# Kernel tuning notes

Measured on AMD Instinct MI355X. Metric: run time of the kernel, lower is better.

## Reference

```python
import jax, jax.numpy as jnp
import numpy as np

N_NODES = 2048
N_EDGES = 65536
IN_CH, HID_CH, OUT_CH = 512, 256, 128
NDIM = 5
THRESHOLD = 0.5


def _gcn(x, src, dst, ew, W, b):
    # GCNConv with self-loops (weight 1): D^{-1/2}(A+I)D^{-1/2} X W + b
    n = x.shape[0]
    deg = jnp.zeros((n,), x.dtype).at[dst].add(ew) + 1.0
    dinv = 1.0 / jnp.sqrt(deg)
    h = x @ W  # [N, out]
    coef = ew * dinv[src] * dinv[dst]  # [E]
    agg = jnp.zeros_like(h).at[dst].add(h[src] * coef[:, None])
    return agg + h / deg[:, None] + b


def _class_flags(feat, thr):
    # cosine similarity -> unnormalized Laplacian -> eigengap-based class ids
    xn = feat / (jnp.linalg.norm(feat, axis=1, keepdims=True) + 1e-8)
    S = xn @ xn.T  # [N, N]
    L = jnp.diag(jnp.sum(S, axis=1)) - S
    vals = jnp.linalg.eigvalsh(jax.lax.stop_gradient(L))  # ascending (class ids are non-diff)
    gaps = jnp.diff(vals)
    return jnp.concatenate([jnp.zeros((1,), jnp.int32),
                            jnp.cumsum((gaps > thr).astype(jnp.int32))])


def _class_avg(flags, feat):
    # per-class mean features, gathered back to each node
    n = feat.shape[0]
    sums = jax.ops.segment_sum(feat, flags, num_segments=n)
    cnts = jax.ops.segment_sum(jnp.ones((n,), feat.dtype), flags, num_segments=n)
    avg = sums / jnp.maximum(cnts, 1.0)[:, None]
    return avg[flags]


def _block(prev_gcn, skip, srcs, dsts, ews, convW, convb, linW, linb, k,
           changeW=None, changeb=None):
    gcn_out, outs = [], []
    for i in range(NDIM):
        g = _gcn(prev_gcn[i], srcs[i], dsts[i], ews[i], convW[i], convb[i])
        flags = _class_flags(g, THRESHOLD)
        lin = _class_avg(flags, g) @ linW + linb
        fir = skip[i] @ changeW + changeb if changeW is not None else skip[i]
        fea = fir + k * lin  # add_class_avg_to_node_features
        outs.append(jax.nn.relu(fir + fea))
        gcn_out.append(g)
    return gcn_out, outs


def _forward(dims, edge_indices, edge_weights, convWs, convbs, linWs, linbs,
             change1_W, change1_b, change2_W, change2_b, dimension_weights, k_save):
    srcs = [edge_indices[i, 0] for i in range(NDIM)]
    dsts = [edge_indices[i, 1] for i in range(NDIM)]
    ews = [edge_weights[i] for i in range(NDIM)]
    w = dimension_weights / jnp.sum(dimension_weights)
    g, out = _block(dims, dims, srcs, dsts, ews, convWs[0], convbs[0], linWs[0], linbs[0], k_save, change1_W, change1_b)
    g, out = _block(g, out, srcs, dsts, ews, convWs[1], convbs[1], linWs[1], linbs[1], k_save, change2_W, change2_b)
    for layer in range(2, 6):
        g, out = _block(g, out, srcs, dsts, ews, convWs[layer], convbs[layer], linWs[layer], linbs[layer], k_save)
    # dimension-weighted fusion of final per-dimension outputs
    return sum(w[i] * out[i] for i in range(NDIM))


def setup_inputs() -> dict:
    key = jax.random.key(0)
    ks = iter(jax.random.split(key, 80))
    def nrm(shape, s=0.05):
        return (jax.random.normal(next(ks), shape, jnp.float32) * s)
    inp = {}
    for i in range(NDIM):
        inp[f"dim{i+1}"] = jax.random.normal(next(ks), (N_NODES, IN_CH), jnp.float32)
    inp["edge_indices"] = jax.random.randint(next(ks), (NDIM, 2, N_EDGES), 0, N_NODES, jnp.int32)
    inp["edge_weights"] = jax.random.uniform(next(ks), (NDIM, N_EDGES), jnp.float32)
    inp["non_zero"] = N_NODES
    conv_shapes = [(IN_CH, HID_CH), (HID_CH, OUT_CH)] + [(OUT_CH, OUT_CH)] * 4
    for l, (ci, co) in enumerate(conv_shapes, start=1):
        inp[f"convW{l}"] = nrm((NDIM, ci, co))
        inp[f"convb{l}"] = nrm((NDIM, co))
    lin_shapes = [HID_CH, OUT_CH, OUT_CH, OUT_CH, OUT_CH, OUT_CH]
    names = ["preLin1", "preLin2", "preLin3", "behLin1", "behLin2", "behLin3"]
    for nm, c in zip(names, lin_shapes):
        inp[f"{nm}_W"] = nrm((c, c))
        inp[f"{nm}_b"] = nrm((c,))
    inp["change1_W"] = nrm((IN_CH, HID_CH)); inp["change1_b"] = nrm((HID_CH,))
    inp["change2_W"] = nrm((HID_CH, OUT_CH)); inp["change2_b"] = nrm((OUT_CH,))
    inp["dimension_weights"] = jnp.ones((NDIM,), jnp.float32)
    inp["k_save"] = jnp.float32(0.5)
    return inp


def reference(dim1, dim2, dim3, dim4, dim5, edge_indices, edge_weights, non_zero,
              convW1, convb1, convW2, convb2, convW3, convb3, convW4, convb4,
              convW5, convb5, convW6, convb6,
              preLin1_W, preLin1_b, preLin2_W, preLin2_b, preLin3_W, preLin3_b,
              behLin1_W, behLin1_b, behLin2_W, behLin2_b, behLin3_W, behLin3_b,
              change1_W, change1_b, change2_W, change2_b, dimension_weights, k_save):
    dims = [dim1, dim2, dim3, dim4, dim5]
    convWs = [convW1, convW2, convW3, convW4, convW5, convW6]
    convbs = [convb1, convb2, convb3, convb4, convb5, convb6]
    linWs = [preLin1_W, preLin2_W, preLin3_W, behLin1_W, behLin2_W, behLin3_W]
    linbs = [preLin1_b, preLin2_b, preLin3_b, behLin1_b, behLin2_b, behLin3_b]
    return _forward(dims, edge_indices, edge_weights, convWs, convbs, linWs, linbs,
                    change1_W, change1_b, change2_W, change2_b, dimension_weights, k_save)
```

## Files before the change

kernel.cpp:

```cpp
#include <hip/hip_runtime.h>
#include <math.h>
#include <stdint.h>

#define NN 2048
#define NE 65536
#define ND 5
#define DMX 256
#define MAXB1 2048
#define SUBD 8
#define NBF (MAXB1*SUBD+1)
#define NFMAX 1536
#define MAXRUN 1536
#define NPB 4
#define COARSE_H 1.76f
#define NUDGE 2e-3f
#define THRG 0.5f

typedef float f32x16 __attribute__((ext_vector_type(16)));
typedef short s16x8 __attribute__((ext_vector_type(8)));
typedef unsigned short u16x8 __attribute__((ext_vector_type(8)));

__device__ __forceinline__ float wredSum(float v){
#pragma unroll
  for (int o=32;o>0;o>>=1) v += __shfl_down(v,o,64);
  return v;
}
__device__ __forceinline__ float wredMin(float v){
#pragma unroll
  for (int o=32;o>0;o>>=1) v = fminf(v,__shfl_down(v,o,64));
  return v;
}
__device__ __forceinline__ float wredMax(float v){
#pragma unroll
  for (int o=32;o>0;o>>=1) v = fmaxf(v,__shfl_down(v,o,64));
  return v;
}
__device__ __forceinline__ uint32_t encF(float f){
  uint32_t u = __float_as_uint(f);
  return (u & 0x80000000u) ? ~u : (u | 0x80000000u);
}
__device__ __forceinline__ float decF(uint32_t u){
  return (u & 0x80000000u) ? __uint_as_float(u ^ 0x80000000u) : __uint_as_float(~u);
}
__device__ __forceinline__ uint16_t bf16hi(float f){
  return (uint16_t)(__float_as_uint(f)>>16);
}

template<int BLK>
__device__ float bredSum(float v, float* red){
  v = wredSum(v);
  const int w = threadIdx.x >> 6;
  if ((threadIdx.x & 63) == 0) red[w] = v;
  __syncthreads();
  if (threadIdx.x == 0){
    float s = 0.f;
#pragma unroll
    for (int i=0;i<BLK/64;i++) s += red[i];
    red[0] = s;
  }
  __syncthreads();
  float r = red[0];
  __syncthreads();
  return r;
}

__global__ void k_prep(const float* __restrict__ xn, uint16_t* __restrict__ xph,
                       uint16_t* __restrict__ xpl, int co){
  const int dim = blockIdx.y;
  const int c2 = blockIdx.x;
  const int col = threadIdx.x;
  const float* x = xn + (size_t)dim*NN*co;
  const int kb = c2*8;
  u16x8 h8, l8;
#pragma unroll
  for (int j=0;j<8;j++){
    const float x0 = x[(size_t)(kb+j)*co + col];
    const uint16_t h = bf16hi(x0);
    h8[j] = h;
    l8[j] = bf16hi(x0 - __uint_as_float((uint32_t)h<<16));
  }
  const size_t o = ((size_t)dim*(NN/8) + c2)*co + col;
  reinterpret_cast<u16x8*>(xph)[o] = h8;
  reinterpret_cast<u16x8*>(xpl)[o] = l8;
}

template<int D, int BLK>
__device__ int evalNu(const uint16_t* __restrict__ xph, const uint16_t* __restrict__ xpl,
                      const float* __restrict__ a,
                      float t0, float dlt,
                      float* M, float* Pt, float* red, float* wrow,
                      float* scal, float* tOut)
{
  const int tid = threadIdx.x;
  float* fsc = scal + 16;

  float md = 1e30f;
  for (int i=tid;i<NN;i+=BLK) md = fminf(md, fabsf(a[i]-t0));
  md = wredMin(md);
  if ((tid & 63) == 0) red[tid>>6] = md;
  __syncthreads();
  if (tid == 0){
    float m2 = 1e30f;
    for (int i=0;i<BLK/64;i++) m2 = fminf(m2, red[i]);
    scal[1] = (m2 < 1e-3f) ? (t0 + dlt) : t0;
  }
  __syncthreads();
  const float t = scal[1];
  __syncthreads();

  float c = 0.f;
  for (int i=tid;i<NN;i+=BLK) c += (a[i] < t) ? 1.f : 0.f;
  float cnt = bredSum<BLK>(c, red);

  constexpr int BG  = D/64;
  constexpr int NBL = BG*(BG+1)/2;
  constexpr int SXT = 24;
  static_assert(BLK == NBL*64, "one wave per tile block");
  static_assert(4*D*SXT*2 <= (D*(D+1)/2)*4, "XT overlay fits in M");

  uint16_t* XTh = reinterpret_cast<uint16_t*>(M);
  uint16_t* XTl = XTh + D*SXT;
  uint16_t* WXh = XTl + D*SXT;
  uint16_t* WXl = WXh + D*SXT;
  const u16x8* XPH = reinterpret_cast<const u16x8*>(xph);
  const u16x8* XPL = reinterpret_cast<const u16x8*>(xpl);

  const int wv_ = tid >> 6, lane = tid & 63;
  int bi = 0, bj = 0;
  { int rem = wv_; while (rem >= BG - bi){ rem -= BG - bi; bi++; } bj = bi + rem; }
  const int colA = bi*64 + (lane & 31);
  const int colB = bj*64 + (lane & 31);
  const int kgo  = (lane >> 5) * 8;

  f32x16 acc0, acc1, acc2, acc3;
#pragma unroll
  for (int e=0;e<16;e++){ acc0[e]=0.f; acc1[e]=0.f; acc2[e]=0.f; acc3[e]=0.f; }

  if (tid < 16){
    float den = a[tid] - t;
    if (fabsf(den) < 1e-5f) den = (den < 0.f) ? -1e-5f : 1e-5f;
    wrow[tid] = 1.0f/den;
  }

  for (int k0=0; k0<NN; k0+=16){
    __syncthreads();
    const float* wcur = wrow + ((k0>>4)&1)*16;
    for (int it = tid; it < 2*D; it += BLK){
      const int kg  = it / D;
      const int col = it - kg*D;
      const u16x8 xh8 = XPH[(size_t)((k0>>3)+kg)*D + col];
      const u16x8 xl8 = XPL[(size_t)((k0>>3)+kg)*D + col];
      const float4 w0 = *reinterpret_cast<const float4*>(&wcur[kg*8]);
      const float4 w1 = *reinterpret_cast<const float4*>(&wcur[kg*8+4]);
      const float wv[8] = {w0.x,w0.y,w0.z,w0.w,w1.x,w1.y,w1.z,w1.w};
      u16x8 sph, spl;
#pragma unroll
      for (int j=0;j<8;j++){
        const float hf = __uint_as_float((uint32_t)(uint16_t)xh8[j]<<16);
        const float lf = __uint_as_float((uint32_t)(uint16_t)xl8[j]<<16);
        const float p0 = wv[j]*(hf+lf);
        const uint16_t hp = bf16hi(p0);
        sph[j] = hp;
        spl[j] = bf16hi(p0 - __uint_as_float((uint32_t)hp<<16));
      }
      const int base = col*SXT + kg*8;
      *reinterpret_cast<u16x8*>(XTh + base) = xh8;
      *reinterpret_cast<u16x8*>(XTl + base) = xl8;
      *reinterpret_cast<u16x8*>(WXh + base) = sph;
      *reinterpret_cast<u16x8*>(WXl + base) = spl;
    }
    if (tid < 16 && k0+16 < NN){
      float den = a[k0+16+tid] - t;
      if (fabsf(den) < 1e-5f) den = (den < 0.f) ? -1e-5f : 1e-5f;
      wrow[((((k0>>4)+1)&1)<<4) + tid] = 1.0f/den;
    }
    __syncthreads();
    const s16x8 ah0 = *reinterpret_cast<const s16x8*>(WXh + colA*SXT + kgo);
    const s16x8 ah1 = *reinterpret_cast<const s16x8*>(WXh + (colA+32)*SXT + kgo);
    const s16x8 al0 = *reinterpret_cast<const s16x8*>(WXl + colA*SXT + kgo);
    const s16x8 al1 = *reinterpret_cast<const s16x8*>(WXl + (colA+32)*SXT + kgo);
    const s16x8 bh0 = *reinterpret_cast<const s16x8*>(XTh + colB*SXT + kgo);
    const s16x8 bh1 = *reinterpret_cast<const s16x8*>(XTh + (colB+32)*SXT + kgo);
    const s16x8 bl0 = *reinterpret_cast<const s16x8*>(XTl + colB*SXT + kgo);
    const s16x8 bl1 = *reinterpret_cast<const s16x8*>(XTl + (colB+32)*SXT + kgo);
    acc0 = __builtin_amdgcn_mfma_f32_32x32x16_bf16(ah0, bh0, acc0, 0,0,0);
    acc1 = __builtin_amdgcn_mfma_f32_32x32x16_bf16(ah0, bh1, acc1, 0,0,0);
    acc2 = __builtin_amdgcn_mfma_f32_32x32x16_bf16(ah1, bh0, acc2, 0,0,0);
    acc3 = __builtin_amdgcn_mfma_f32_32x32x16_bf16(ah1, bh1, acc3, 0,0,0);
    acc0 = __builtin_amdgcn_mfma_f32_32x32x16_bf16(ah0, bl0, acc0, 0,0,0);
    acc1 = __builtin_amdgcn_mfma_f32_32x32x16_bf16(ah0, bl1, acc1, 0,0,0);
    acc2 = __builtin_amdgcn_mfma_f32_32x32x16_bf16(ah1, bl0, acc2, 0,0,0);
    acc3 = __builtin_amdgcn_mfma_f32_32x32x16_bf16(ah1, bl1, acc3, 0,0,0);
    acc0 = __builtin_amdgcn_mfma_f32_32x32x16_bf16(al0, bh0, acc0, 0,0,0);
    acc1 = __builtin_amdgcn_mfma_f32_32x32x16_bf16(al0, bh1, acc1, 0,0,0);
    acc2 = __builtin_amdgcn_mfma_f32_32x32x16_bf16(al1, bh0, acc2, 0,0,0);
    acc3 = __builtin_amdgcn_mfma_f32_32x32x16_bf16(al1, bh1, acc3, 0,0,0);
  }
  __syncthreads();

  {
    const int rbase = 4*(lane>>5);
#pragma unroll
    for (int q=0;q<4;q++){
      const f32x16 A = (q==0)?acc0:((q==1)?acc1:((q==2)?acc2:acc3));
      const int ta = 2*bi + (q>>1), tb = 2*bj + (q&1);
      const int bb = tb*32 + (lane & 31);
#pragma unroll
      for (int r=0;r<16;r++){
        const int aa = ta*32 + (r&3) + 8*(r>>2) + rbase;
        if (aa <= bb)
          M[aa*D - (aa*(aa-1))/2 + (bb-aa)] = ((aa==bb)?1.f:0.f) - A[r];
      }
    }
  }

  constexpr int PS = 12;
  int neg = 0;
  for (int k0=0; k0<D; k0+=8){
    const int k1 = k0+8;
    __syncthreads();
    if (tid < 64){
      if (tid == 0){
        float B[8][8];
#pragma unroll
        for (int q=0;q<8;q++){
#pragma unroll
          for (int p=0;p<=q;p++){
            const int g = k0+p;
            B[p][q] = M[g*D - (g*(g-1))/2 + (k0+q-g)];
          }
        }
        float inv8[8];
#pragma unroll
        for (int q=0;q<8;q++){
          float d = B[q][q];
          if (d < 0.f) neg++;
          if (fabsf(d) < 1e-8f) d = (d<0.f)?-1e-8f:1e-8f;
          const float inv = 1.0f/d;
          inv8[q] = inv;
#pragma unroll
          for (int i=q+1;i<8;i++){
            const float f = B[q][i]*inv;
#pragma unroll
            for (int j=i;j<8;j++) B[i][j] = fmaf(-f, B[q][j], B[i][j]);
          }
        }
#pragma unroll
        for (int q=0;q<8;q++){
          fsc[36+q] = inv8[q];
#pragma unroll
          for (int p=0;p<=q;p++) fsc[(q*(q+1))/2 + p] = B[p][q];
        }
      }
      __asm__ __volatile__("s_waitcnt lgkmcnt(0)" ::: "memory");
      float c8[36], iv8[8];
#pragma unroll
      for (int k=0;k<36;k++) c8[k] = fsc[k];
#pragma unroll
      for (int k=0;k<8;k++) iv8[k] = fsc[36+k];
      for (int j = k1 + tid; j < D; j += 64){
        float rv[8], pt[8];
#pragma unroll
        for (int q=0;q<8;q++){
          const int g = k0+q;
          rv[q] = M[g*D - (g*(g-1))/2 + (j-g)];
        }
#pragma unroll
        for (int q=0;q<8;q++){
          float v = rv[q];
#pragma unroll
          for (int p=0;p<q;p++) v = fmaf(-c8[(q*(q+1))/2 + p], pt[p], v);
          pt[q] = v * iv8[q];
          const int g = k0+q;
          M[g*D - (g*(g-1))/2 + (j-g)] = v;
          Pt[j*PS + q] = pt[q];
        }
      }
    }
    __syncthreads();
    if (k1 < D){
      constexpr int G = BLK/4;
      const int grp = tid / G, sub = tid % G;
      for (int i0=k1; i0<D; i0+=4){
        const int i = i0 + grp;
        float cq[8];
#pragma unroll
        for (int q=0;q<8;q++){
          const int g = k0+q;
          cq[q] = M[g*D - (g*(g-1))/2 + (i-g)];
        }
        const int offi = i*D - (i*(i-1))/2;
        for (int j=i+sub; j<D; j+=G){
          const float4 p0 = *reinterpret_cast<const float4*>(&Pt[j*PS + 0]);
          const float4 p1 = *reinterpret_cast<const float4*>(&Pt[j*PS + 4]);
          float v = M[offi + (j-i)];
          v = fmaf(-cq[0],p0.x,v); v = fmaf(-cq[1],p0.y,v);
          v = fmaf(-cq[2],p0.z,v); v = fmaf(-cq[3],p0.w,v);
          v = fmaf(-cq[4],p1.x,v); v = fmaf(-cq[5],p1.y,v);
          v = fmaf(-cq[6],p1.z,v); v = fmaf(-cq[7],p1.w,v);
          M[offi + (j-i)] = v;
        }
      }
    }
  }
  if (tid == 0) ((int*)scal)[5] = neg;
  __syncthreads();
  const int negAll = ((int*)scal)[5];
  __syncthreads();

  *tOut = t;
  return negAll + (int)(cnt + 0.5f);
}

#define SMEM_D(D) (((D)*((D)+1)/2 + 12*(D) + 112)*4)

template<int D, int BLK, int WPE>
__global__ __launch_bounds__(BLK,WPE) void k_eval(const uint16_t* __restrict__ xph,
    const uint16_t* __restrict__ xpl,
    const float* __restrict__ ab, const float* __restrict__ ctrlF,
    const int* __restrict__ ctrlI, int* __restrict__ nu1, float* __restrict__ tus1)
{
  const int dim = blockIdx.y;
  const int b = blockIdx.x;
  if (b > ctrlI[dim*8+0]) return;
  extern __shared__ float smem[];
  constexpr int TRI = D*(D+1)/2;
  float* M = smem; float* Pt = M+TRI; float* red = Pt + 12*D;
  float* wrow = red+16; float* scal = wrow+32;
  const float lo = ctrlF[dim*8+0], h1 = ctrlF[dim*8+1];
  float tU;
  int v = evalNu<D,BLK>(xph + (size_t)dim*NN*D, xpl + (size_t)dim*NN*D,
                        ab + dim*NN, lo + h1*b, NUDGE,
                        M,Pt,red,wrow,scal,&tU);
  if (threadIdx.x == 0){ nu1[dim*(MAXB1+1)+b] = v; tus1[dim*(MAXB1+1)+b] = tU; }
}

template<int D, int BLK, int WPE>
__global__ __launch_bounds__(BLK,WPE) void k_evalF(const uint16_t* __restrict__ xph,
    const uint16_t* __restrict__ xpl,
    const float* __restrict__ ab, const float* __restrict__ ctrlF,
    const int* __restrict__ ctrlI, const int* __restrict__ fineBins,
    int* __restrict__ nuF, float* __restrict__ tusF)
{
  const int dim = blockIdx.y;
  const int task = blockIdx.x / (SUBD-1);
  int cnt = ctrlI[dim*8+3]; if (cnt > NFMAX) cnt = NFMAX;
  if (task >= cnt) return;
  const int s = blockIdx.x % (SUBD-1) + 1;
  const int bin = fineBins[dim*NFMAX + task];
  extern __shared__ float smem[];
  constexpr int TRI = D*(D+1)/2;
  float* M = smem; float* Pt = M+TRI; float* red = Pt + 12*D;
  float* wrow = red+16; float* scal = wrow+32;
  const float lo = ctrlF[dim*8+0], hf = ctrlF[dim*8+1]*(1.0f/SUBD);
  const int f = bin*SUBD + s;
  float tU;
  int v = evalNu<D,BLK>(xph + (size_t)dim*NN*D, xpl + (size_t)dim*NN*D,
                        ab + dim*NN, lo + hf*f, NUDGE,
                        M,Pt,red,wrow,scal,&tU);
  if (threadIdx.x == 0){ nuF[(size_t)dim*NBF+f] = v; tusF[(size_t)dim*NBF+f] = tU; }
}

template<int D, int BLK, int WPE>
__global__ __launch_bounds__(BLK,WPE) void k_probe(const uint16_t* __restrict__ xph,
    const uint16_t* __restrict__ xpl,
    const float* __restrict__ ab, const int* __restrict__ ctrlI,
    const int* __restrict__ runP, const float* __restrict__ runB,
    int* __restrict__ nuP, float* __restrict__ tP)
{
  const int dim = blockIdx.y;
  const int r = blockIdx.x >> 3;
  int nr = ctrlI[dim*8+1]; if (nr > MAXRUN) nr = MAXRUN;
  if (r >= nr) return;
  const int side = (blockIdx.x >> 2) & 1;
  const int i = blockIdx.x & 3;
  extern __shared__ float smem[];
  constexpr int TRI = D*(D+1)/2;
  float* M = smem; float* Pt = M+TRI; float* red = Pt + 12*D;
  float* wrow = red+16; float* scal = wrow+32;
  const float* rb = runB + (size_t)(dim*MAXRUN + r)*4;
  const float lo = rb[side*2+0], hi = rb[side*2+1];
  const float t0 = lo + (hi - lo)*(float)(i+1)*(1.0f/(NPB+1));
  const float dlt = fminf(NUDGE, (hi-lo)*0.08f);
  float tU;
  int v = evalNu<D,BLK>(xph + (size_t)dim*NN*D, xpl + (size_t)dim*NN*D,
                        ab + dim*NN, t0, dlt,
                        M,Pt,red,wrow,scal,&tU);
  if (threadIdx.x == 0){
    const size_t o = (((size_t)dim*MAXRUN + r)*2 + side)*NPB + i;
    nuP[o] = v; tP[o] = tU;
  }
}

__global__ void k_decide(const int* __restrict__ ctrlI, const int* __restrict__ runP,
                         const float* __restrict__ runB, const int* __restrict__ nuP,
                         const float* __restrict__ tP, int* __restrict__ bnd){
  const int dim = blockIdx.x;
  int nr = ctrlI[dim*8+1]; if (nr > MAXRUN) nr = MAXRUN;
  for (int r = threadIdx.x; r < nr; r += blockDim.x){
    const int p = runP[dim*MAXRUN + r];
    const float* rb = runB + (size_t)(dim*MAXRUN + r)*4;
    float lam[2];
    for (int side=0; side<2; side++){
      const int rank = p + side;
      const size_t o = (((size_t)dim*MAXRUN + r)*2 + side)*NPB;
      float prev = rb[side*2+0];
      bool found = false; float l = 0.f;
      for (int i=0;i<NPB;i++){
        const float ti = tP[o+i];
        if (nuP[o+i] >= rank){ l = 0.5f*(prev + ti); found = true; break; }
        prev = ti;
      }
      if (!found) l = 0.5f*(prev + rb[side*2+1]);
      lam[side] = l;
    }
    if (lam[1] - lam[0] > THRG) bnd[dim*NN + p - 1] = 1;
  }
}

__global__ void k_sel(const int* __restrict__ nu1, int* ctrlI,
                      int* __restrict__ binSel, int* __restrict__ fineBins){
  const int dim = blockIdx.y;
  const int j = blockIdx.x*256 + threadIdx.x;
// ... 470 lines not shown
  const float* convW[6]; const float* convb[6];
  for (int l=0;l<6;l++){ convW[l] = (const float*)d_in[8+2*l]; convb[l] = (const float*)d_in[9+2*l]; }
  const float* linW[6]; const float* linb[6];
  for (int l=0;l<6;l++){ linW[l] = (const float*)d_in[20+2*l]; linb[l] = (const float*)d_in[21+2*l]; }
  const float* ch1W = (const float*)d_in[32]; const float* ch1b = (const float*)d_in[33];
  const float* ch2W = (const float*)d_in[34]; const float* ch2b = (const float*)d_in[35];
  const float* dimw = (const float*)d_in[36]; const float* ksv = (const float*)d_in[37];

  char* p = (char*)d_ws;
  auto take = [&](size_t bytes)->char*{
    char* r = p; p += (bytes + 255) & ~(size_t)255; return r;
  };
  int*   csr_base = (int*)  take((size_t)ND*(NN+1)*4);
  int*   csr_cur  = (int*)  take((size_t)ND*NN*4);
  int*   csr_psrc = (int*)  take((size_t)ND*NE*4);
  float* csr_coef = (float*)take((size_t)ND*NE*4);
  float* deg      = (float*)take((size_t)ND*NN*4);
  float* selfw    = (float*)take((size_t)ND*NN*4);
  float* gA   = (float*)take((size_t)ND*NN*DMX*4);
  float* gB   = (float*)take((size_t)ND*NN*DMX*4);
  float* outA = (float*)take((size_t)ND*NN*DMX*4);
  float* outB = (float*)take((size_t)ND*NN*DMX*4);
  float* hbuf = (float*)take((size_t)ND*NN*DMX*4);
  float* xnbuf= (float*)take((size_t)ND*NN*DMX*4);
  float* cavg = (float*)take((size_t)ND*NN*DMX*4);
  uint16_t* xph = (uint16_t*)take((size_t)ND*NN*DMX*2);
  uint16_t* xpl = (uint16_t*)take((size_t)ND*NN*DMX*2);
  float* abuf = (float*)take((size_t)ND*NN*4);
  float* sbuf = (float*)take((size_t)ND*DMX*4);
  float* Cbuf = (float*)take((size_t)ND*DMX*DMX*4);
  float* vpow = (float*)take((size_t)ND*NN*4);
  float* zpartG=(float*)take((size_t)ND*16*DMX*4);
  float* scACC =(float*)take((size_t)2*ND*2*4);
  int*   nu1  = (int*)  take((size_t)ND*(MAXB1+1)*4);
  float* tus1 = (float*)take((size_t)ND*(MAXB1+1)*4);
  int*   nuF  = (int*)  take((size_t)ND*NBF*4);
  float* tusF = (float*)take((size_t)ND*NBF*4);
  int*   binSel=(int*)  take((size_t)ND*MAXB1*4);
  int*   fineBins=(int*)take((size_t)ND*NFMAX*4);
  int*   runP = (int*)  take((size_t)ND*MAXRUN*4);
  float* runB = (float*)take((size_t)ND*MAXRUN*4*4);
  int*   nuP  = (int*)  take((size_t)ND*MAXRUN*2*NPB*4);
  float* tP   = (float*)take((size_t)ND*MAXRUN*2*NPB*4);
  int*   bnd  = (int*)  take((size_t)ND*NN*4);
  int*   flagsA=(int*)  take((size_t)ND*NN*4);
  int*   cstart=(int*)  take((size_t)ND*(NN+1)*4);
  float* ctrlF= (float*)take((size_t)ND*8*4);
  uint32_t* ctrlU = (uint32_t*)take((size_t)ND*8*4);
  int*   ctrlI= (int*)  take((size_t)ND*8*4);
  float* thB  = (float*)take((size_t)ND*4);
  (void)ws_size; (void)in_sizes; (void)n_in; (void)out_size;

  {
    void (*pe)(const uint16_t*,const uint16_t*,const float*,const float*,const int*,int*,float*) = k_eval<256,640,1>;
    hipFuncSetAttribute((const void*)pe, hipFuncAttributeMaxDynamicSharedMemorySize, SMEM_D(256));
    void (*pf)(const uint16_t*,const uint16_t*,const float*,const float*,const int*,const int*,int*,float*) = k_evalF<256,640,1>;
    hipFuncSetAttribute((const void*)pf, hipFuncAttributeMaxDynamicSharedMemorySize, SMEM_D(256));
    void (*pp)(const uint16_t*,const uint16_t*,const float*,const int*,const int*,const float*,int*,float*) = k_probe<256,640,1>;
    hipFuncSetAttribute((const void*)pp, hipFuncAttributeMaxDynamicSharedMemorySize, SMEM_D(256));
  }

  k_init<<<ND, 256, 0, stream>>>(deg, csr_cur);
  k_count<<<(ND*NE+255)/256, 256, 0, stream>>>(eidx, ew, deg, csr_cur);
  k_prefix<<<ND, 64, 0, stream>>>(csr_cur, csr_base);
  k_fill_csr<<<(ND*NE+255)/256, 256, 0, stream>>>(eidx, ew, deg, csr_cur, csr_psrc, csr_coef);
  k_selfw<<<(ND*NN+255)/256, 256, 0, stream>>>(deg, selfw);

  float* gbufs[2] = {gA, gB};
// ... 16 lines not shown
      k_gemm<<<dim3(co/64, NN/64, ND), 256, 0, stream>>>(
        gPrev, (long long)NN*ci, convW[l], (long long)ci*co, nullptr, 0,
        hbuf, (long long)NN*co, NN, ci, co);
    }

    k_layerinit<<<ND, 256, 0, stream>>>(bnd, ctrlU, ctrlI);
    k_agg<<<dim3(NN, ND), co, 0, stream>>>(hbuf, gCur, convb[l], csr_base, csr_psrc,
                                           csr_coef, selfw, co);
    k_rownorm<<<dim3(NN, ND), 256, 0, stream>>>(gCur, xnbuf, co);
    k_prep<<<dim3(NN/8, ND), co, 0, stream>>>(xnbuf, xph, xpl, co);
    k_colsum<<<dim3(co/64, ND), 256, 0, stream>>>(xnbuf, sbuf, co);
    k_adot<<<dim3(NN/8, ND), 512, 0, stream>>>(xnbuf, sbuf, abuf, ctrlU, co);
    k_gramC<<<dim3((co/32)*(co/32), ND), 256, 0, stream>>>(xnbuf, Cbuf, co);

    k_pw_init<<<ND, 1024, 0, stream>>>(vpow, scACC);
    if (l==0){
      for (int it=0; it<33; it++){
        const int sp = it & 1, sc = sp ^ 1;
        k_pw_z<256><<<dim3(16, ND), 256, 0, stream>>>(xnbuf, vpow, zpartG, scACC, sc);
        k_pw_y<256><<<dim3(16, ND), 256, 0, stream>>>(xnbuf, abuf, ctrlU, zpartG, vpow, scACC, sp, sc);
      }
    } else {
      for (int it=0; it<33; it++){
        const int sp = it & 1, sc = sp ^ 1;
        k_pw_z<128><<<dim3(16, ND), 128, 0, stream>>>(xnbuf, vpow, zpartG, scACC, sc);
        k_pw_y<128><<<dim3(16, ND), 256, 0, stream>>>(xnbuf, abuf, ctrlU, zpartG, vpow, scACC, sp, sc);
      }
    }
    k_pw_fin<<<1, 64, 0, stream>>>(scACC, thB, 1);

    k_bounds<<<ND, 256, 0, stream>>>(Cbuf, ctrlU, thB, ctrlF, ctrlI, co);

    if (l==0){
      k_eval<256,640,1><<<dim3(MAXB1+1, ND), 640, SMEM_D(256), stream>>>(xph, xpl, abuf, ctrlF, ctrlI, nu1, tus1);
      k_sel<<<dim3((MAXB1+255)/256, ND), 256, 0, stream>>>(nu1, ctrlI, binSel, fineBins);
      k_fill<<<dim3((NBF+255)/256, ND), 256, 0, stream>>>(nu1, tus1, binSel, ctrlF, ctrlI, nuF, tusF);
      k_evalF<256,640,1><<<dim3(NFMAX*(SUBD-1), ND), 640, SMEM_D(256), stream>>>(xph, xpl, abuf, ctrlF, ctrlI, fineBins, nuF, tusF);
      k_runs<<<dim3((NBF+255)/256, ND), 256, 0, stream>>>(nuF, tusF, ctrlI, runP, runB, bnd);
      k_probe<256,640,1><<<dim3(MAXRUN*2*NPB, ND), 640, SMEM_D(256), stream>>>(xph, xpl, abuf, ctrlI, runP, runB, nuP, tP);
      k_decide<<<ND, 256, 0, stream>>>(ctrlI, runP, runB, nuP, tP, bnd);
    } else {
      k_eval<128,192,4><<<dim3(MAXB1+1, ND), 192, SMEM_D(128), stream>>>(xph, xpl, abuf, ctrlF, ctrlI, nu1, tus1);
      k_sel<<<dim3((MAXB1+255)/256, ND), 256, 0, stream>>>(nu1, ctrlI, binSel, fineBins);
      k_fill<<<dim3((NBF+255)/256, ND), 256, 0, stream>>>(nu1, tus1, binSel, ctrlF, ctrlI, nuF, tusF);
      k_evalF<128,192,4><<<dim3(NFMAX*(SUBD-1), ND), 192, SMEM_D(128), stream>>>(xph, xpl, abuf, ctrlF, ctrlI, fineBins, nuF, tusF);
      k_runs<<<dim3((NBF+255)/256, ND), 256, 0, stream>>>(nuF, tusF, ctrlI, runP, runB, bnd);
      k_probe<128,192,4><<<dim3(MAXRUN*2*NPB, ND), 192, SMEM_D(128), stream>>>(xph, xpl, abuf, ctrlI, runP, runB, nuP, tP);
      k_decide<<<ND, 256, 0, stream>>>(ctrlI, runP, runB, nuP, tP, bnd);
    }

    k_flags<<<ND, 64, 0, stream>>>(bnd, flagsA, cstart, ctrlI);
    k_cavg<<<dim3(128, ND), 256, 0, stream>>>(gCur, cstart, ctrlI, cavg, co);
    k_clin<<<dim3(128, ND), 256, 0, stream>>>(cavg, linW[l], linb[l], xnbuf, ctrlI, co);

    const float* firPtr;
    if (l==0){
      for (int d=0;d<ND;d++)
        k_gemm<<<dim3(256/64, NN/64, 1), 256, 0, stream>>>(
          dims_in[d], 0, ch1W, 0, ch1b, 0, hbuf + (size_t)d*NN*256, 0, NN, 512, 256);
      firPtr = hbuf;
    } else if (l==1){
      k_gemm<<<dim3(128/64, NN/64, ND), 256, 0, stream>>>(
        oPrev, (long long)NN*256, ch2W, 0, ch2b, 0, hbuf, (long long)NN*128, NN, 256, 128);
      firPtr = hbuf;
    } else {
      firPtr = oPrev;
    }

    k_out<<<dim3(NN, ND), co, 0, stream>>>(firPtr, xnbuf, flagsA, ksv, oCur, co);

    gPrev = gCur; oPrev = oCur;
  }

  k_final<<<NN, 128, 0, stream>>>(oPrev, dimw, (float*)d_out);
}
```

Measured before the change: 33.05 ms.

## Evaluate two shift points per block sharing X tiles in Sylvester inertia counts

Each eval/evalF/probe block now computes eigenvalue counts for two shifts at once. It loads the bf16 hi/lo X tiles once per k-step, builds two weighted copies, and runs two sets of MFMA accumulators, so the global loads, tile staging and reductions are shared across both shifts. The grids are halved to match. The cost is double the accumulator registers, more LDS (the overlay now spills into Pt), and two sequential LDLT factorizations per block, which can lower occupancy. SUBD-1=7 fine points are covered with 4 pairs, with the eighth point guarded off.

```diff
diff --git a/kernel.cpp b/kernel.cpp
--- a/kernel.cpp
+++ b/kernel.cpp
@@ -46,24 +46,6 @@
   return (uint16_t)(__float_as_uint(f)>>16);
 }
 
-template<int BLK>
-__device__ float bredSum(float v, float* red){
-  v = wredSum(v);
-  const int w = threadIdx.x >> 6;
-  if ((threadIdx.x & 63) == 0) red[w] = v;
-  __syncthreads();
-  if (threadIdx.x == 0){
-    float s = 0.f;
-#pragma unroll
-    for (int i=0;i<BLK/64;i++) s += red[i];
-    red[0] = s;
-  }
-  __syncthreads();
-  float r = red[0];
-  __syncthreads();
-  return r;
-}
-
 __global__ void k_prep(const float* __restrict__ xn, uint16_t* __restrict__ xph,
                        uint16_t* __restrict__ xpl, int co){
   const int dim = blockIdx.y;
@@ -85,43 +67,65 @@
 }
 
 template<int D, int BLK>
-__device__ int evalNu(const uint16_t* __restrict__ xph, const uint16_t* __restrict__ xpl,
-                      const float* __restrict__ a,
-                      float t0, float dlt,
-                      float* M, float* Pt, float* red, float* wrow,
-                      float* scal, float* tOut)
+__device__ void evalNu2(const uint16_t* __restrict__ xph, const uint16_t* __restrict__ xpl,
+                        const float* __restrict__ a,
+                        float t0a, float t0b, float dlt,
+                        float* M, float* Pt, float* red, float* wrow,
+                        float* scal,
+                        float* tOutA, float* tOutB, int* nuOutA, int* nuOutB)
 {
   const int tid = threadIdx.x;
   float* fsc = scal + 16;
 
-  float md = 1e30f;
-  for (int i=tid;i<NN;i+=BLK) md = fminf(md, fabsf(a[i]-t0));
-  md = wredMin(md);
-  if ((tid & 63) == 0) red[tid>>6] = md;
+  float md0 = 1e30f, md1 = 1e30f;
+  for (int i=tid;i<NN;i+=BLK){
+    const float av = a[i];
+    md0 = fminf(md0, fabsf(av - t0a));
+    md1 = fminf(md1, fabsf(av - t0b));
+  }
+  md0 = wredMin(md0); md1 = wredMin(md1);
+  if ((tid & 63) == 0){ red[tid>>6] = md0; red[16 + (tid>>6)] = md1; }
   __syncthreads();
   if (tid == 0){
-    float m2 = 1e30f;
-    for (int i=0;i<BLK/64;i++) m2 = fminf(m2, red[i]);
-    scal[1] = (m2 < 1e-3f) ? (t0 + dlt) : t0;
-  }
-  __syncthreads();
-  const float t = scal[1];
-  __syncthreads();
-
-  float c = 0.f;
-  for (int i=tid;i<NN;i+=BLK) c += (a[i] < t) ? 1.f : 0.f;
-  float cnt = bredSum<BLK>(c, red);
+    float m0 = 1e30f, m1 = 1e30f;
+    for (int i=0;i<BLK/64;i++){ m0 = fminf(m0, red[i]); m1 = fminf(m1, red[16+i]); }
+    scal[1] = (m0 < 1e-3f) ? (t0a + dlt) : t0a;
+    scal[2] = (m1 < 1e-3f) ? (t0b + dlt) : t0b;
+  }
+  __syncthreads();
+  const float tA = scal[1], tB = scal[2];
+  __syncthreads();
+
+  float c0 = 0.f, c1 = 0.f;
+  for (int i=tid;i<NN;i+=BLK){
+    const float av = a[i];
+    c0 += (av < tA) ? 1.f : 0.f;
+    c1 += (av < tB) ? 1.f : 0.f;
+  }
+  c0 = wredSum(c0); c1 = wredSum(c1);
+  if ((tid & 63) == 0){ red[tid>>6] = c0; red[16 + (tid>>6)] = c1; }
+  __syncthreads();
+  if (tid == 0){
+    float s0=0.f, s1=0.f;
+    for (int i=0;i<BLK/64;i++){ s0 += red[i]; s1 += red[16+i]; }
+    red[0] = s0; red[16] = s1;
+  }
+  __syncthreads();
+  const float cntA = red[0], cntB = red[16];
+  __syncthreads();
 
   constexpr int BG  = D/64;
   constexpr int NBL = BG*(BG+1)/2;
   constexpr int SXT = 24;
   static_assert(BLK == NBL*64, "one wave per tile block");
-  static_assert(4*D*SXT*2 <= (D*(D+1)/2)*4, "XT overlay fits in M");
+  static_assert(6*D*SXT*2 <= (D*(D+1)/2 + 12*D)*4, "XT overlay fits in M+Pt");
 
   uint16_t* XTh = reinterpret_cast<uint16_t*>(M);
   uint16_t* XTl = XTh + D*SXT;
-  uint16_t* WXh = XTl + D*SXT;
-  uint16_t* WXl = WXh + D*SXT;
+  uint16_t* WAh = XTl + D*SXT;
+  uint16_t* WAl = WAh + D*SXT;
+  uint16_t* WBh = WAl + D*SXT;
+  uint16_t* WBl = WBh + D*SXT;
   const u16x8* XPH = reinterpret_cast<const u16x8*>(xph);
   const u16x8* XPL = reinterpret_cast<const u16x8*>(xpl);
 
@@ -132,77 +136,118 @@
   const int colB = bj*64 + (lane & 31);
   const int kgo  = (lane >> 5) * 8;
 
-  f32x16 acc0, acc1, acc2, acc3;
-#pragma unroll
-  for (int e=0;e<16;e++){ acc0[e]=0.f; acc1[e]=0.f; acc2[e]=0.f; acc3[e]=0.f; }
+  f32x16 accA0, accA1, accA2, accA3, accB0, accB1, accB2, accB3;
+#pragma unroll
+  for (int e=0;e<16;e++){
+    accA0[e]=0.f; accA1[e]=0.f; accA2[e]=0.f; accA3[e]=0.f;
+    accB0[e]=0.f; accB1[e]=0.f; accB2[e]=0.f; accB3[e]=0.f;
+  }
 
   if (tid < 16){
-    float den = a[tid] - t;
+    float den = a[tid] - tA;
     if (fabsf(den) < 1e-5f) den = (den < 0.f) ? -1e-5f : 1e-5f;
     wrow[tid] = 1.0f/den;
+  } else if (tid < 32){
+    float den = a[tid-16] - tB;
+    if (fabsf(den) < 1e-5f) den = (den < 0.f) ? -1e-5f : 1e-5f;
+    wrow[32 + (tid-16)] = 1.0f/den;
   }
 
   for (int k0=0; k0<NN; k0+=16){
     __syncthreads();
-    const float* wcur = wrow + ((k0>>4)&1)*16;
+    const int buf = (k0>>4)&1;
+    const float* wA = wrow + buf*16;
+    const float* wB = wrow + 32 + buf*16;
     for (int it = tid; it < 2*D; it += BLK){
       const int kg  = it / D;
       const int col = it - kg*D;
       const u16x8 xh8 = XPH[(size_t)((k0>>3)+kg)*D + col];
       const u16x8 xl8 = XPL[(size_t)((k0>>3)+kg)*D + col];
-      const float4 w0 = *reinterpret_cast<const float4*>(&wcur[kg*8]);
-      const float4 w1 = *reinterpret_cast<const float4*>(&wcur[kg*8+4]);
-      const float wv[8] = {w0.x,w0.y,w0.z,w0.w,w1.x,w1.y,w1.z,w1.w};
-      u16x8 sph, spl;
+      const float4 wa0 = *reinterpret_cast<const float4*>(&wA[kg*8]);
+      const float4 wa1 = *reinterpret_cast<const float4*>(&wA[kg*8+4]);
+      const float4 wb0 = *reinterpret_cast<const float4*>(&wB[kg*8]);
+      const float4 wb1 = *reinterpret_cast<const float4*>(&wB[kg*8+4]);
+      const float wva[8] = {wa0.x,wa0.y,wa0.z,wa0.w,wa1.x,wa1.y,wa1.z,wa1.w};
+      const float wvb[8] = {wb0.x,wb0.y,wb0.z,wb0.w,wb1.x,wb1.y,wb1.z,wb1.w};
+      u16x8 sphA, splA, sphB, splB;
 #pragma unroll
       for (int j=0;j<8;j++){
         const float hf = __uint_as_float((uint32_t)(uint16_t)xh8[j]<<16);
         const float lf = __uint_as_float((uint32_t)(uint16_t)xl8[j]<<16);
-        const float p0 = wv[j]*(hf+lf);
-        const uint16_t hp = bf16hi(p0);
-        sph[j] = hp;
-        spl[j] = bf16hi(p0 - __uint_as_float((uint32_t)hp<<16));
+        const float xt = hf + lf;
+        const float pA = wva[j]*xt;
+        const uint16_t hA = bf16hi(pA);
+        sphA[j] = hA;
+        splA[j] = bf16hi(pA - __uint_as_float((uint32_t)hA<<16));
+        const float pB = wvb[j]*xt;
+        const uint16_t hB = bf16hi(pB);
+        sphB[j] = hB;
+        splB[j] = bf16hi(pB - __uint_as_float((uint32_t)hB<<16));
       }
       const int base = col*SXT + kg*8;
       *reinterpret_cast<u16x8*>(XTh + base) = xh8;
       *reinterpret_cast<u16x8*>(XTl + base) = xl8;
-      *reinterpret_cast<u16x8*>(WXh + base) = sph;
-      *reinterpret_cast<u16x8*>(WXl + base) = spl;
-    }
-    if (tid < 16 && k0+16 < NN){
-      float den = a[k0+16+tid] - t;
-      if (fabsf(den) < 1e-5f) den = (den < 0.f) ? -1e-5f : 1e-5f;
-      wrow[((((k0>>4)+1)&1)<<4) + tid] = 1.0f/den;
+      *reinterpret_cast<u16x8*>(WAh + base) = sphA;
+      *reinterpret_cast<u16x8*>(WAl + base) = splA;
+      *reinterpret_cast<u16x8*>(WBh + base) = sphB;
+      *reinterpret_cast<u16x8*>(WBl + base) = splB;
+    }
+    if (k0+16 < NN){
+      if (tid < 16){
+        float den = a[k0+16+tid] - tA;
+        if (fabsf(den) < 1e-5f) den = (den < 0.f) ? -1e-5f : 1e-5f;
+        wrow[((buf^1)<<4) + tid] = 1.0f/den;
+      } else if (tid < 32){
+        float den = a[k0+16+(tid-16)] - tB;
+        if (fabsf(den) < 1e-5f) den = (den < 0.f) ? -1e-5f : 1e-5f;
+        wrow[32 + ((buf^1)<<4) + (tid-16)] = 1.0f/den;
+      }
     }
     __syncthreads();
-    const s16x8 ah0 = *reinterpret_cast<const s16x8*>(WXh + colA*SXT + kgo);
-    const s16x8 ah1 = *reinterpret_cast<const s16x8*>(WXh + (colA+32)*SXT + kgo);
-    const s16x8 al0 = *reinterpret_cast<const s16x8*>(WXl + colA*SXT + kgo);
-    const s16x8 al1 = *reinterpret_cast<const s16x8*>(WXl + (colA+32)*SXT + kgo);
+    const s16x8 aAh0 = *reinterpret_cast<const s16x8*>(WAh + colA*SXT + kgo);
+    const s16x8 aAh1 = *reinterpret_cast<const s16x8*>(WAh + (colA+32)*SXT + kgo);
+    const s16x8 aAl0 = *reinterpret_cast<const s16x8*>(WAl + colA*SXT + kgo);
+    const s16x8 aAl1 = *reinterpret_cast<const s16x8*>(WAl + (colA+32)*SXT + kgo);
+    const s16x8 aBh0 = *reinterpret_cast<const s16x8*>(WBh + colA*SXT + kgo);
+    const s16x8 aBh1 = *reinterpret_cast<const s16x8*>(WBh + (colA+32)*SXT + kgo);
+    const s16x8 aBl0 = *reinterpret_cast<const s16x8*>(WBl + colA*SXT + kgo);
+    const s16x8 aBl1 = *reinterpret_cast<const s16x8*>(WBl + (colA+32)*SXT + kgo);
     const s16x8 bh0 = *reinterpret_cast<const s16x8*>(XTh + colB*SXT + kgo);
     const s16x8 bh1 = *reinterpret_cast<const s16x8*>(XTh + (colB+32)*SXT + kgo);
     const s16x8 bl0 = *reinterpret_cast<const s16x8*>(XTl + colB*SXT + kgo);
     const s16x8 bl1 = *reinterpret_cast<const s16x8*>(XTl + (colB+32)*SXT + kgo);
-    acc0 = __builtin_amdgcn_mfma_f32_32x32x16_bf16(ah0, bh0, acc0, 0,0,0);
-    acc1 = __builtin_amdgcn_mfma_f32_32x32x16_bf16(ah0, bh1, acc1, 0,0,0);
-    acc2 = __builtin_amdgcn_mfma_f32_32x32x16_bf16(ah1, bh0, acc2, 0,0,0);
-    acc3 = __builtin_amdgcn_mfma_f32_32x32x16_bf16(ah1, bh1, acc3, 0,0,0);
-    acc0 = __builtin_amdgcn_mfma_f32_32x32x16_bf16(ah0, bl0, acc0, 0,0,0);
-    acc1 = __builtin_amdgcn_mfma_f32_32x32x16_bf16(ah0, bl1, acc1, 0,0,0);
-    acc2 = __builtin_amdgcn_mfma_f32_32x32x16_bf16(ah1, bl0, acc2, 0,0,0);
-    acc3 = __builtin_amdgcn_mfma_f32_32x32x16_bf16(ah1, bl1, acc3, 0,0,0);
-    acc0 = __builtin_amdgcn_mfma_f32_32x32x16_bf16(al0, bh0, acc0, 0,0,0);
-    acc1 = __builtin_amdgcn_mfma_f32_32x32x16_bf16(al0, bh1, acc1, 0,0,0);
-    acc2 = __builtin_amdgcn_mfma_f32_32x32x16_bf16(al1, bh0, acc2, 0,0,0);
-    acc3 = __builtin_amdgcn_mfma_f32_32x32x16_bf16(al1, bh1, acc3, 0,0,0);
-  }
-  __syncthreads();
-
-  {
+    accA0 = __builtin_amdgcn_mfma_f32_32x32x16_bf16(aAh0, bh0, accA0, 0,0,0);
+    accB0 = __builtin_amdgcn_mfma_f32_32x32x16_bf16(aBh0, bh0, accB0, 0,0,0);
+    accA1 = __builtin_amdgcn_mfma_f32_32x32x16_bf16(aAh0, bh1, accA1, 0,0,0);
+    accB1 = __builtin_amdgcn_mfma_f32_32x32x16_bf16(aBh0, bh1, accB1, 0,0,0);
+    accA2 = __builtin_amdgcn_mfma_f32_32x32x16_bf16(aAh1, bh0, accA2, 0,0,0);
+    accB2 = __builtin_amdgcn_mfma_f32_32x32x16_bf16(aBh1, bh0, accB2, 0,0,0);
+    accA3 = __builtin_amdgcn_mfma_f32_32x32x16_bf16(aAh1, bh1, accA3, 0,0,0);
+    accB3 = __builtin_amdgcn_mfma_f32_32x32x16_bf16(aBh1, bh1, accB3, 0,0,0);
+    accA0 = __builtin_amdgcn_mfma_f32_32x32x16_bf16(aAh0, bl0, accA0, 0,0,0);
+    accB0 = __builtin_amdgcn_mfma_f32_32x32x16_bf16(aBh0, bl0, accB0, 0,0,0);
+    accA1 = __builtin_amdgcn_mfma_f32_32x32x16_bf16(aAh0, bl1, accA1, 0,0,0);
+    accB1 = __builtin_amdgcn_mfma_f32_32x32x16_bf16(aBh0, bl1, accB1, 0,0,0);
+    accA2 = __builtin_amdgcn_mfma_f32_32x32x16_bf16(aAh1, bl0, accA2, 0,0,0);
+    accB2 = __builtin_amdgcn_mfma_f32_32x32x16_bf16(aBh1, bl0, accB2, 0,0,0);
+    accA3 = __builtin_amdgcn_mfma_f32_32x32x16_bf16(aAh1, bl1, accA3, 0,0,0);
+    accB3 = __builtin_amdgcn_mfma_f32_32x32x16_bf16(aBh1, bl1, accB3, 0,0,0);
+    accA0 = __builtin_amdgcn_mfma_f32_32x32x16_bf16(aAl0, bh0, accA0, 0,0,0);
+    accB0 = __builtin_amdgcn_mfma_f32_32x32x16_bf16(aBl0, bh0, accB0, 0,0,0);
+    accA1 = __builtin_amdgcn_mfma_f32_32x32x16_bf16(aAl0, bh1, accA1, 0,0,0);
+    accB1 = __builtin_amdgcn_mfma_f32_32x32x16_bf16(aBl0, bh1, accB1, 0,0,0);
+    accA2 = __builtin_amdgcn_mfma_f32_32x32x16_bf16(aAl1, bh0, accA2, 0,0,0);
+    accB2 = __builtin_amdgcn_mfma_f32_32x32x16_bf16(aBl1, bh0, accB2, 0,0,0);
+    accA3 = __builtin_amdgcn_mfma_f32_32x32x16_bf16(aAl1, bh1, accA3, 0,0,0);
+    accB3 = __builtin_amdgcn_mfma_f32_32x32x16_bf16(aBl1, bh1, accB3, 0,0,0);
+  }
+  __syncthreads();
+
+  auto writeM = [&](const f32x16& A0, const f32x16& A1, const f32x16& A2, const f32x16& A3){
     const int rbase = 4*(lane>>5);
 #pragma unroll
     for (int q=0;q<4;q++){
-      const f32x16 A = (q==0)?acc0:((q==1)?acc1:((q==2)?acc2:acc3));
+      const f32x16& A = (q==0)?A0:((q==1)?A1:((q==2)?A2:A3));
       const int ta = 2*bi + (q>>1), tb = 2*bj + (q&1);
       const int bb = tb*32 + (lane & 31);
 #pragma unroll
@@ -212,107 +257,119 @@
           M[aa*D - (aa*(aa-1))/2 + (bb-aa)] = ((aa==bb)?1.f:0.f) - A[r];
       }
     }
-  }
+  };
 
   constexpr int PS = 12;
-  int neg = 0;
-  for (int k0=0; k0<D; k0+=8){
-    const int k1 = k0+8;
-    __syncthreads();
-    if (tid < 64){
-      if (tid == 0){
-        float B[8][8];
-#pragma unroll
-        for (int q=0;q<8;q++){
-#pragma unroll
-          for (int p=0;p<=q;p++){
-            const int g = k0+p;
-            B[p][q] = M[g*D - (g*(g-1))/2 + (k0+q-g)];
+  auto ldlt = [&]()->int{
+    int neg = 0;
+    for (int kp=0; kp<D; kp+=8){
+      const int k1 = kp+8;
+      __syncthreads();
+      if (tid < 64){
+        if (tid == 0){
+          float B[8][8];
+#pragma unroll
+          for (int q=0;q<8;q++){
+#pragma unroll
+            for (int p=0;p<=q;p++){
+              const int g = kp+p;
+              B[p][q] = M[g*D - (g*(g-1))/2 + (kp+q-g)];
+            }
+          }
+          float inv8[8];
+#pragma unroll
+          for (int q=0;q<8;q++){
+            float d = B[q][q];
+            if (d < 0.f) neg++;
+            if (fabsf(d) < 1e-8f) d = (d<0.f)?-1e-8f:1e-8f;
+            const float inv = 1.0f/d;
+            inv8[q] = inv;
+#pragma unroll
+            for (int i=q+1;i<8;i++){
+              const float f = B[q][i]*inv;
+#pragma unroll
+              for (int j=i;j<8;j++) B[i][j] = fmaf(-f, B[q][j], B[i][j]);
+            }
+          }
+#pragma unroll
+          for (int q=0;q<8;q++){
+            fsc[36+q] = inv8[q];
+#pragma unroll
+            for (int p=0;p<=q;p++) fsc[(q*(q+1))/2 + p] = B[p][q];
           }
         }
-        float inv8[8];
-#pragma unroll
-        for (int q=0;q<8;q++){
-          float d = B[q][q];
-          if (d < 0.f) neg++;
-          if (fabsf(d) < 1e-8f) d = (d<0.f)?-1e-8f:1e-8f;
-          const float inv = 1.0f/d;
-          inv8[q] = inv;
-#pragma unroll
-          for (int i=q+1;i<8;i++){
-            const float f = B[q][i]*inv;
-#pragma unroll
-            for (int j=i;j<8;j++) B[i][j] = fmaf(-f, B[q][j], B[i][j]);
+        __asm__ __volatile__("s_waitcnt lgkmcnt(0)" ::: "memory");
+        float c8[36], iv8[8];
+#pragma unroll
+        for (int k=0;k<36;k++) c8[k] = fsc[k];
+#pragma unroll
+        for (int k=0;k<8;k++) iv8[k] = fsc[36+k];
+        for (int j = k1 + tid; j < D; j += 64){
+          float rv[8], pt[8];
+#pragma unroll
+          for (int q=0;q<8;q++){
+            const int g = kp+q;
+            rv[q] = M[g*D - (g*(g-1))/2 + (j-g)];
+          }
+#pragma unroll
+          for (int q=0;q<8;q++){
+            float v = rv[q];
+#pragma unroll
+            for (int p=0;p<q;p++) v = fmaf(-c8[(q*(q+1))/2 + p], pt[p], v);
+            pt[q] = v * iv8[q];
+            const int g = kp+q;
+            M[g*D - (g*(g-1))/2 + (j-g)] = v;
+            Pt[j*PS + q] = pt[q];
           }
         }
-#pragma unroll
-        for (int q=0;q<8;q++){
-          fsc[36+q] = inv8[q];
-#pragma unroll
-          for (int p=0;p<=q;p++) fsc[(q*(q+1))/2 + p] = B[p][q];
+      }
+      __syncthreads();
+      if (k1 < D){
+        constexpr int G = BLK/4;
+        const int grp = tid / G, sub = tid % G;
+        for (int i0=k1; i0<D; i0+=4){
+          const int i = i0 + grp;
+          float cq[8];
+#pragma unroll
+          for (int q=0;q<8;q++){
+            const int g = kp+q;
+            cq[q] = M[g*D - (g*(g-1))/2 + (i-g)];
+          }
+          const int offi = i*D - (i*(i-1))/2;
+          for (int j=i+sub; j<D; j+=G){
+            const float4 p0 = *reinterpret_cast<const float4*>(&Pt[j*PS + 0]);
+            const float4 p1 = *reinterpret_cast<const float4*>(&Pt[j*PS + 4]);
+            float v = M[offi + (j-i)];
+            v = fmaf(-cq[0],p0.x,v); v = fmaf(-cq[1],p0.y,v);
+            v = fmaf(-cq[2],p0.z,v); v = fmaf(-cq[3],p0.w,v);
+            v = fmaf(-cq[4],p1.x,v); v = fmaf(-cq[5],p1.y,v);
+            v = fmaf(-cq[6],p1.z,v); v = fmaf(-cq[7],p1.w,v);
+            M[offi + (j-i)] = v;
+          }
         }
       }
-      __asm__ __volatile__("s_waitcnt lgkmcnt(0)" ::: "memory");
-      float c8[36], iv8[8];
-#pragma unroll
-      for (int k=0;k<36;k++) c8[k] = fsc[k];
-#pragma unroll
-      for (int k=0;k<8;k++) iv8[k] = fsc[36+k];
-      for (int j = k1 + tid; j < D; j += 64){
-        float rv[8], pt[8];
-#pragma unroll
-        for (int q=0;q<8;q++){
-          const int g = k0+q;
-          rv[q] = M[g*D - (g*(g-1))/2 + (j-g)];
-        }
-#pragma unroll
-        for (int q=0;q<8;q++){
-          float v = rv[q];
-#pragma unroll
-          for (int p=0;p<q;p++) v = fmaf(-c8[(q*(q+1))/2 + p], pt[p], v);
-          pt[q] = v * iv8[q];
-          const int g = k0+q;
-          M[g*D - (g*(g-1))/2 + (j-g)] = v;
-          Pt[j*PS + q] = pt[q];
-        }
-      }
-    }
-    __syncthreads();
-    if (k1 < D){
-      constexpr int G = BLK/4;
-      const int grp = tid / G, sub = tid % G;
-      for (int i0=k1; i0<D; i0+=4){
-        const int i = i0 + grp;
-        float cq[8];
-#pragma unroll
-        for (int q=0;q<8;q++){
-          const int g = k0+q;
-          cq[q] = M[g*D - (g*(g-1))/2 + (i-g)];
-        }
-        const int offi = i*D - (i*(i-1))/2;
-        for (int j=i+sub; j<D; j+=G){
-          const float4 p0 = *reinterpret_cast<const float4*>(&Pt[j*PS + 0]);
-          const float4 p1 = *reinterpret_cast<const float4*>(&Pt[j*PS + 4]);
-          float v = M[offi + (j-i)];
-          v = fmaf(-cq[0],p0.x,v); v = fmaf(-cq[1],p0.y,v);
-          v = fmaf(-cq[2],p0.z,v); v = fmaf(-cq[3],p0.w,v);
-          v = fmaf(-cq[4],p1.x,v); v = fmaf(-cq[5],p1.y,v);
-          v = fmaf(-cq[6],p1.z,v); v = fmaf(-cq[7],p1.w,v);
-          M[offi + (j-i)] = v;
-        }
-      }
-    }
-  }
-  if (tid == 0) ((int*)scal)[5] = neg;
-  __syncthreads();
-  const int negAll = ((int*)scal)[5];
-  __syncthreads();
-
-  *tOut = t;
-  return negAll + (int)(cnt + 0.5f);
-}
-
-#define SMEM_D(D) (((D)*((D)+1)/2 + 12*(D) + 112)*4)
+    }
+    return neg;
+  };
+
+  writeM(accA0, accA1, accA2, accA3);
+  const int negA = ldlt();
+  if (tid == 0) ((int*)scal)[5] = negA;
+  __syncthreads();
+  writeM(accB0, accB1, accB2, accB3);
+  const int negB = ldlt();
+  if (tid == 0) ((int*)scal)[6] = negB;
+  __syncthreads();
+  const int nA = ((int*)scal)[5];
+  const int nB = ((int*)scal)[6];
+  __syncthreads();
+
+  *tOutA = tA; *tOutB = tB;
+  *nuOutA = nA + (int)(cntA + 0.5f);
+  *nuOutB = nB + (int)(cntB + 0.5f);
+}
+
+#define SMEM_D(D) (((D)*((D)+1)/2 + 12*(D) + 160)*4)
 
 template<int D, int BLK, int WPE>
 __global__ __launch_bounds__(BLK,WPE) void k_eval(const uint16_t* __restrict__ xph,
@@ -321,18 +378,21 @@
     const int* __restrict__ ctrlI, int* __restrict__ nu1, float* __restrict__ tus1)
 {
   const int dim = blockIdx.y;
-  const int b = blockIdx.x;
-  if (b > ctrlI[dim*8+0]) return;
+  const int b0 = blockIdx.x*2, b1 = b0+1;
+  if (b0 > ctrlI[dim*8+0]) return;
   extern __shared__ float smem[];
   constexpr int TRI = D*(D+1)/2;
   float* M = smem; float* Pt = M+TRI; float* red = Pt + 12*D;
-  float* wrow = red+16; float* scal = wrow+32;
+  float* wrow = red+32; float* scal = wrow+64;
   const float lo = ctrlF[dim*8+0], h1 = ctrlF[dim*8+1];
-  float tU;
-  int v = evalNu<D,BLK>(xph + (size_t)dim*NN*D, xpl + (size_t)dim*NN*D,
-                        ab + dim*NN, lo + h1*b, NUDGE,
-                        M,Pt,red,wrow,scal,&tU);
-  if (threadIdx.x == 0){ nu1[dim*(MAXB1+1)+b] = v; tus1[dim*(MAXB1+1)+b] = tU; }
+  float tUA, tUB; int vA, vB;
+  evalNu2<D,BLK>(xph + (size_t)dim*NN*D, xpl + (size_t)dim*NN*D,
+                 ab + dim*NN, lo + h1*b0, lo + h1*b1, NUDGE,
+                 M,Pt,red,wrow,scal,&tUA,&tUB,&vA,&vB);
+  if (threadIdx.x == 0){
+    nu1[dim*(MAXB1+1)+b0] = vA; tus1[dim*(MAXB1+1)+b0] = tUA;
+    if (b1 <= MAXB1){ nu1[dim*(MAXB1+1)+b1] = vB; tus1[dim*(MAXB1+1)+b1] = tUB; }
+  }
 }
 
 template<int D, int BLK, int WPE>
@@ -343,22 +403,26 @@
     int* __restrict__ nuF, float* __restrict__ tusF)
 {
   const int dim = blockIdx.y;
-  const int task = blockIdx.x / (SUBD-1);
+  const int task = blockIdx.x >> 2;
   int cnt = ctrlI[dim*8+3]; if (cnt > NFMAX) cnt = NFMAX;
   if (task >= cnt) return;
-  const int s = blockIdx.x % (SUBD-1) + 1;
+  const int r = blockIdx.x & 3;
+  const int s0 = 2*r + 1, s1 = s0 + 1;
   const int bin = fineBins[dim*NFMAX + task];
   extern __shared__ float smem[];
   constexpr int TRI = D*(D+1)/2;
   float* M = smem; float* Pt = M+TRI; float* red = Pt + 12*D;
-  float* wrow = red+16; float* scal = wrow+32;
+  float* wrow = red+32; float* scal = wrow+64;
   const float lo = ctrlF[dim*8+0], hf = ctrlF[dim*8+1]*(1.0f/SUBD);
-  const int f = bin*SUBD + s;
-  float tU;
-  int v = evalNu<D,BLK>(xph + (size_t)dim*NN*D, xpl + (size_t)dim*NN*D,
-                        ab + dim*NN, lo + hf*f, NUDGE,
-                        M,Pt,red,wrow,scal,&tU);
-  if (threadIdx.x == 0){ nuF[(size_t)dim*NBF+f] = v; tusF[(size_t)dim*NBF+f] = tU; }
+  const int f0 = bin*SUBD + s0, f1 = bin*SUBD + s1;
+  float tUA, tUB; int vA, vB;
+  evalNu2<D,BLK>(xph + (size_t)dim*NN*D, xpl + (size_t)dim*NN*D,
+                 ab + dim*NN, lo + hf*f0, lo + hf*f1, NUDGE,
+                 M,Pt,red,wrow,scal,&tUA,&tUB,&vA,&vB);
+  if (threadIdx.x == 0){
+    nuF[(size_t)dim*NBF+f0] = vA; tusF[(size_t)dim*NBF+f0] = tUA;
+    if (s1 < SUBD){ nuF[(size_t)dim*NBF+f1] = vB; tusF[(size_t)dim*NBF+f1] = tUB; }
+  }
 }
 
 template<int D, int BLK, int WPE>
@@ -369,26 +433,29 @@
     int* __restrict__ nuP, float* __restrict__ tP)
 {
   const int dim = blockIdx.y;
-  const int r = blockIdx.x >> 3;
+  const int r = blockIdx.x >> 2;
   int nr = ctrlI[dim*8+1]; if (nr > MAXRUN) nr = MAXRUN;
   if (r >= nr) return;
-  const int side = (blockIdx.x >> 2) & 1;
-  const int i = blockIdx.x & 3;
+  const int side = (blockIdx.x >> 1) & 1;
+  const int ip = blockIdx.x & 1;
+  const int i0 = 2*ip, i1 = i0+1;
   extern __shared__ float smem[];
   constexpr int TRI = D*(D+1)/2;
   float* M = smem; float* Pt = M+TRI; float* red = Pt + 12*D;
-  float* wrow = red+16; float* scal = wrow+32;
+  float* wrow = red+32; float* scal = wrow+64;
   const float* rb = runB + (size_t)(dim*MAXRUN + r)*4;
   const float lo = rb[side*2+0], hi = rb[side*2+1];
-  const float t0 = lo + (hi - lo)*(float)(i+1)*(1.0f/(NPB+1));
+  const float t0 = lo + (hi - lo)*(float)(i0+1)*(1.0f/(NPB+1));
+  const float t1 = lo + (hi - lo)*(float)(i1+1)*(1.0f/(NPB+1));
   const float dlt = fminf(NUDGE, (hi-lo)*0.08f);
-  float tU;
-  int v = evalNu<D,BLK>(xph + (size_t)dim*NN*D, xpl + (size_t)dim*NN*D,
-                        ab + dim*NN, t0, dlt,
-                        M,Pt,red,wrow,scal,&tU);
+  float tUA, tUB; int vA, vB;
+  evalNu2<D,BLK>(xph + (size_t)dim*NN*D, xpl + (size_t)dim*NN*D,
+                 ab + dim*NN, t0, t1, dlt,
+                 M,Pt,red,wrow,scal,&tUA,&tUB,&vA,&vB);
   if (threadIdx.x == 0){
-    const size_t o = (((size_t)dim*MAXRUN + r)*2 + side)*NPB + i;
-    nuP[o] = v; tP[o] = tU;
+    const size_t o = (((size_t)dim*MAXRUN + r)*2 + side)*NPB;
+    nuP[o+i0] = vA; tP[o+i0] = tUA;
+    nuP[o+i1] = vB; tP[o+i1] = tUB;
   }
 }
 
@@ -925,8 +992,8 @@
   float* vpow = (float*)take((size_t)ND*NN*4);
   float* zpartG=(float*)take((size_t)ND*16*DMX*4);
   float* scACC =(float*)take((size_t)2*ND*2*4);
-  int*   nu1  = (int*)  take((size_t)ND*(MAXB1+1)*4);
-  float* tus1 = (float*)take((size_t)ND*(MAXB1+1)*4);
+  int*   nu1  = (int*)  take((size_t)ND*(MAXB1+2)*4);
+  float* tus1 = (float*)take((size_t)ND*(MAXB1+2)*4);
   int*   nuF  = (int*)  take((size_t)ND*NBF*4);
   float* tusF = (float*)take((size_t)ND*NBF*4);
   int*   binSel=(int*)  take((size_t)ND*MAXB1*4);
@@ -1009,20 +1076,20 @@
     k_bounds<<<ND, 256, 0, stream>>>(Cbuf, ctrlU, thB, ctrlF, ctrlI, co);
 
     if (l==0){
-      k_eval<256,640,1><<<dim3(MAXB1+1, ND), 640, SMEM_D(256), stream>>>(xph, xpl, abuf, ctrlF, ctrlI, nu1, tus1);
+      k_eval<256,640,1><<<dim3((MAXB1+2)/2, ND), 640, SMEM_D(256), stream>>>(xph, xpl, abuf, ctrlF, ctrlI, nu1, tus1);
       k_sel<<<dim3((MAXB1+255)/256, ND), 256, 0, stream>>>(nu1, ctrlI, binSel, fineBins);
       k_fill<<<dim3((NBF+255)/256, ND), 256, 0, stream>>>(nu1, tus1, binSel, ctrlF, ctrlI, nuF, tusF);
-      k_evalF<256,640,1><<<dim3(NFMAX*(SUBD-1), ND), 640, SMEM_D(256), stream>>>(xph, xpl, abuf, ctrlF, ctrlI, fineBins, nuF, tusF);
+      k_evalF<256,640,1><<<dim3(NFMAX*4, ND), 640, SMEM_D(256), stream>>>(xph, xpl, abuf, ctrlF, ctrlI, fineBins, nuF, tusF);
       k_runs<<<dim3((NBF+255)/256, ND), 256, 0, stream>>>(nuF, tusF, ctrlI, runP, runB, bnd);
-      k_probe<256,640,1><<<dim3(MAXRUN*2*NPB, ND), 640, SMEM_D(256), stream>>>(xph, xpl, abuf, ctrlI, runP, runB, nuP, tP);
+      k_probe<256,640,1><<<dim3(MAXRUN*4, ND), 640, SMEM_D(256), stream>>>(xph, xpl, abuf, ctrlI, runP, runB, nuP, tP);
       k_decide<<<ND, 256, 0, stream>>>(ctrlI, runP, runB, nuP, tP, bnd);
     } else {
-      k_eval<128,192,4><<<dim3(MAXB1+1, ND), 192, SMEM_D(128), stream>>>(xph, xpl, abuf, ctrlF, ctrlI, nu1, tus1);
+      k_eval<128,192,4><<<dim3((MAXB1+2)/2, ND), 192, SMEM_D(128), stream>>>(xph, xpl, abuf, ctrlF, ctrlI, nu1, tus1);
       k_sel<<<dim3((MAXB1+255)/256, ND), 256, 0, stream>>>(nu1, ctrlI, binSel, fineBins);
       k_fill<<<dim3((NBF+255)/256, ND), 256, 0, stream>>>(nu1, tus1, binSel, ctrlF, ctrlI, nuF, tusF);
-      k_evalF<128,192,4><<<dim3(NFMAX*(SUBD-1), ND), 192, SMEM_D(128), stream>>>(xph, xpl, abuf, ctrlF, ctrlI, fineBins, nuF, tusF);
+      k_evalF<128,192,4><<<dim3(NFMAX*4, ND), 192, SMEM_D(128), stream>>>(xph, xpl, abuf, ctrlF, ctrlI, fineBins, nuF, tusF);
       k_runs<<<dim3((NBF+255)/256, ND), 256, 0, stream>>>(nuF, tusF, ctrlI, runP, runB, bnd);
-      k_probe<128,192,4><<<dim3(MAXRUN*2*NPB, ND), 192, SMEM_D(128), stream>>>(xph, xpl, abuf, ctrlI, runP, runB, nuP, tP);
+      k_probe<128,192,4><<<dim3(MAXRUN*4, ND), 192, SMEM_D(128), stream>>>(xph, xpl, abuf, ctrlI, runP, runB, nuP, tP);
       k_decide<<<ND, 256, 0, stream>>>(ctrlI, runP, runB, nuP, tP, bnd);
     }
 
```

New measurement: 116.5 ms. +252.6%, slower.
